# Optimization experiments

Measured on AMD Instinct MI355X. Metric: run time of the kernel, lower is better.

## Reference

```python
import jax, jax.numpy as jnp
import numpy as np

N_NODES = 100000
N_EDGES = 1600000
IN_C, HID_C, OUT_C = 256, 128, 64


def sage_conv(x, src, dst, Wl, Wr, b, n_nodes):
    """PyG SAGEConv: lin_l(mean of neighbor messages) + lin_r(x) + b."""
    msgs = x[src]  # [E, C] gather
    agg = jax.ops.segment_sum(msgs, dst, num_segments=n_nodes)  # [N, C] scatter-add
    deg = jax.ops.segment_sum(jnp.ones((src.shape[0],), x.dtype), dst, num_segments=n_nodes)
    agg = agg / jnp.maximum(deg, 1.0)[:, None]  # mean aggregation, safe for isolated nodes
    return agg @ Wl + x @ Wr + b


def setup_inputs() -> dict:
    key = jax.random.key(0)
    ks = jax.random.split(key, 12)

    def glorot(k, shape):
        fan_in, fan_out = shape
        lim = float(np.sqrt(6.0 / (fan_in + fan_out)))
        return jax.random.uniform(k, shape, jnp.float32, -lim, lim)

    x = jax.random.normal(ks[0], (N_NODES, IN_C), jnp.float32)
    edge_index = jax.random.randint(ks[1], (2, N_EDGES), 0, N_NODES, jnp.int32)
    return {
        "x": x,
        "edge_index": edge_index,
        "Wl0": glorot(ks[2], (IN_C, HID_C)),
        "Wr0": glorot(ks[3], (IN_C, HID_C)),
        "b0": jnp.zeros((HID_C,), jnp.float32),
        "Wl1": glorot(ks[4], (HID_C, HID_C)),
        "Wr1": glorot(ks[5], (HID_C, HID_C)),
        "b1": jnp.zeros((HID_C,), jnp.float32),
        "Wl2": glorot(ks[6], (HID_C, OUT_C)),
        "Wr2": glorot(ks[7], (HID_C, OUT_C)),
        "b2": jnp.zeros((OUT_C,), jnp.float32),
    }


def reference(x, edge_index, Wl0, Wr0, b0, Wl1, Wr1, b1, Wl2, Wr2, b2):
    src, dst = edge_index[0], edge_index[1]
    n = x.shape[0]
    h = x
    out = None
    # convs[:-1]: conv -> relu -> dropout (eval mode: dropout = identity)
    for Wl, Wr, b in ((Wl0, Wr0, b0), (Wl1, Wr1, b1)):
        out = sage_conv(h, src, dst, Wl, Wr, b, n)
        h = jax.nn.relu(out)
    g = h
    x_final = sage_conv(g, src, dst, Wl2, Wr2, b2, n)
    return (x_final, out, g)
```

## Files before the change

kernel.cpp:

```cpp
#include <hip/hip_runtime.h>
#include <stdint.h>

typedef __attribute__((ext_vector_type(4))) float f32x4;
typedef _Float16 half8 __attribute__((ext_vector_type(8)));
typedef _Float16 half4 __attribute__((ext_vector_type(4)));


#define BIN_CHUNK 8192
#define MAXB 512

__global__ __launch_bounds__(256) void k_bhist(const int* __restrict__ dst,
                                               int* __restrict__ bcnt, int E) {
    __shared__ int lh[MAXB];
    for (int i = threadIdx.x; i < MAXB; i += 256) lh[i] = 0;
    __syncthreads();
    const int base = blockIdx.x * BIN_CHUNK;
#pragma unroll 4
    for (int i = 0; i < BIN_CHUNK / 256; i++) {
        int e = base + i * 256 + threadIdx.x;
        if (e < E) atomicAdd(&lh[dst[e] >> 8], 1);
    }
    __syncthreads();
    for (int i = threadIdx.x; i < MAXB; i += 256)
        if (lh[i]) atomicAdd(&bcnt[i], lh[i]);
}

__global__ __launch_bounds__(512) void k_pscan(const int* __restrict__ in,
                                               int* __restrict__ out0,
                                               int* __restrict__ out1,
                                               int* __restrict__ tot, int n) {
    __shared__ int sh[512];
    const int t = threadIdx.x;
    int v[4];
    int s = 0;
#pragma unroll
    for (int i = 0; i < 4; i++) {
        int idx = t * 4 + i;
        v[i] = (idx < n) ? in[idx] : 0;
        s += v[i];
    }
    sh[t] = s;
    __syncthreads();
    for (int off = 1; off < 512; off <<= 1) {
        int add = (t >= off) ? sh[t - off] : 0;
        __syncthreads();
        sh[t] += add;
        __syncthreads();
    }
    int excl = sh[t] - s;
#pragma unroll
    for (int i = 0; i < 4; i++) {
        int idx = t * 4 + i;
        if (idx < n) {
            out0[idx] = excl;
            if (out1) out1[idx] = excl;
        }
        excl += v[i];
    }
    if (t == 511 && tot) *tot = sh[511];
}

__global__ __launch_bounds__(256) void k_bin(const int* __restrict__ src,
                                             const int* __restrict__ dst,
                                             int* __restrict__ gcur,
                                             unsigned* __restrict__ ebuf, int E) {
    __shared__ int lh[MAXB];
    __shared__ int lcur[MAXB];
    for (int i = threadIdx.x; i < MAXB; i += 256) lh[i] = 0;
    __syncthreads();
    const int base = blockIdx.x * BIN_CHUNK;
#pragma unroll 4
    for (int i = 0; i < BIN_CHUNK / 256; i++) {
        int e = base + i * 256 + threadIdx.x;
        if (e < E) atomicAdd(&lh[dst[e] >> 8], 1);
    }
    __syncthreads();
    for (int i = threadIdx.x; i < MAXB; i += 256)
        lcur[i] = lh[i] ? atomicAdd(&gcur[i], lh[i]) : 0;
    __syncthreads();
#pragma unroll 4
    for (int i = 0; i < BIN_CHUNK / 256; i++) {
        int e = base + i * 256 + threadIdx.x;
        if (e < E) {
            int d = dst[e];
            int pos = atomicAdd(&lcur[d >> 8], 1);
            ebuf[pos] = (unsigned)src[e] | ((unsigned)(d & 255) << 24);
        }
    }
}

__global__ __launch_bounds__(256) void k_csr(const unsigned* __restrict__ ebuf,
                                             const int* __restrict__ bbase,
                                             int* __restrict__ rowptr,
                                             int* __restrict__ ssrc, int N) {
    __shared__ int cnt[256];
    __shared__ int sh[256];
    __shared__ int lc[256];
    const int t = threadIdx.x;
    const int b = blockIdx.x;
    cnt[t] = 0;
    __syncthreads();
    const int lo = bbase[b], hi = bbase[b + 1];
    for (int e = lo + t; e < hi; e += 256)
        atomicAdd(&cnt[ebuf[e] >> 24], 1);
    __syncthreads();
    const int myc = cnt[t];
    sh[t] = myc;
    __syncthreads();
    for (int off = 1; off < 256; off <<= 1) {
        int add = (t >= off) ? sh[t - off] : 0;
        __syncthreads();
        sh[t] += add;
        __syncthreads();
    }
    const int base = lo + (sh[t] - myc);
    const int n = (b << 8) + t;
    if (n <= N) rowptr[n] = base;
    lc[t] = base;
    __syncthreads();
    for (int e = lo + t; e < hi; e += 256) {
        unsigned v = ebuf[e];
        int pos = atomicAdd(&lc[v >> 24], 1);
        ssrc[pos] = (int)(v & 0xFFFFFFu);
    }
}


template <int K, int NCOLT>
__device__ inline void wprep_one(const float* __restrict__ Wl, const float* __restrict__ Wr,
                                 _Float16* __restrict__ Wt, int i) {
    constexpr int NCOL = NCOLT / 2;
    int n = i / K, k = i - n * K;
    float v = (n < NCOL) ? Wl[(size_t)k * NCOL + n] : Wr[(size_t)k * NCOL + (n - NCOL)];
    Wt[(size_t)(k >> 5) * (NCOLT * 32) + n * 32 + (k & 31)] = (_Float16)v;
}

__global__ __launch_bounds__(256) void k_wprepAll(
    const float* __restrict__ Wl0, const float* __restrict__ Wr0,
    const float* __restrict__ Wl1, const float* __restrict__ Wr1,
    const float* __restrict__ Wl2, const float* __restrict__ Wr2,
    _Float16* __restrict__ Wt0, _Float16* __restrict__ Wt1, _Float16* __restrict__ Wt2) {
    int i = blockIdx.x * 256 + threadIdx.x;
    if (i < 65536) wprep_one<256, 256>(Wl0, Wr0, Wt0, i);
    else if (i < 98304) wprep_one<128, 256>(Wl1, Wr1, Wt1, i - 65536);
    else if (i < 114688) wprep_one<128, 128>(Wl2, Wr2, Wt2, i - 98304);
}


template <int K, int NCOLT, bool AF32>
__global__ __launch_bounds__(256) void k_gemmM(const void* __restrict__ Av,
                                               const _Float16* __restrict__ Wt,
                                               const float* __restrict__ bias,
                                               _Float16* __restrict__ Cl,
                                               _Float16* __restrict__ Cr, int M) {
    constexpr int NCOL = NCOLT / 2;
    constexpr int WC = NCOLT / 4;
    constexpr int NT = WC / 16;
    constexpr int AS = K + 8;
    constexpr int CS = NCOLT + 8;
    constexpr int MAXS = (K > NCOLT ? K : NCOLT) + 8;
    __shared__ _Float16 sh[64 * MAXS];

    const int tid = threadIdx.x;
    const int lane = tid & 63;
    const int wave = tid >> 6;
    const int quad = lane >> 4;
    const int l16 = lane & 15;
    const int m0 = blockIdx.x * 64;
    const int colbase = wave * WC;

    if (AF32) {
        const float* A = (const float*)Av;
#pragma unroll
        for (int i = 0; i < K / 16; i++) {
            int off = i * 1024 + tid * 4;
            int row = off / K, col = off % K;
            f32x4 u = {0.f, 0.f, 0.f, 0.f};
            if (m0 + row < M) u = *(const f32x4*)(A + (size_t)(m0 + row) * K + col);
            half4 h = {(_Float16)u[0], (_Float16)u[1], (_Float16)u[2], (_Float16)u[3]};
            *(half4*)(sh + row * AS + col) = h;
        }
    } else {
        const _Float16* A = (const _Float16*)Av;
#pragma unroll
        for (int i = 0; i < K / 32; i++) {
            int off = i * 2048 + tid * 8;
            int row = off / K, col = off % K;
            half8 u = {0, 0, 0, 0, 0, 0, 0, 0};
            if (m0 + row < M) u = *(const half8*)(A + (size_t)(m0 + row) * K + col);
            *(half8*)(sh + row * AS + col) = u;
        }
    }
    __syncthreads();

    f32x4 acc[4][NT];
#pragma unroll
    for (int rg = 0; rg < 4; rg++)
#pragma unroll
        for (int t = 0; t < NT; t++) acc[rg][t] = (f32x4){0.f, 0.f, 0.f, 0.f};

#pragma unroll
    for (int k0 = 0; k0 < K; k0 += 32) {
        half8 a[4];
#pragma unroll
        for (int rg = 0; rg < 4; rg++)
            a[rg] = *(const half8*)(sh + (rg * 16 + l16) * AS + k0 + quad * 8);
        half8 b[NT];
        const _Float16* Wk = Wt + (size_t)(k0 >> 5) * (NCOLT * 32);
#pragma unroll
        for (int t = 0; t < NT; t++)
            b[t] = *(const half8*)(Wk + (colbase + t * 16 + l16) * 32 + quad * 8);
#pragma unroll
        for (int rg = 0; rg < 4; rg++)
#pragma unroll
            for (int t = 0; t < NT; t++)
                acc[rg][t] = __builtin_amdgcn_mfma_f32_16x16x32_f16(b[t], a[rg], acc[rg][t], 0, 0, 0);
    }

    __syncthreads();

#pragma unroll
    for (int t = 0; t < NT; t++) {
        int c0 = colbase + t * 16 + quad * 4;
        f32x4 bv = {0.f, 0.f, 0.f, 0.f};
        if (c0 >= NCOL) bv = *(const f32x4*)(bias + (c0 - NCOL));
#pragma unroll
        for (int rg = 0; rg < 4; rg++) {
            half4 h = {(_Float16)(acc[rg][t][0] + bv[0]), (_Float16)(acc[rg][t][1] + bv[1]),
                       (_Float16)(acc[rg][t][2] + bv[2]), (_Float16)(acc[rg][t][3] + bv[3])};
            *(half4*)(sh + (rg * 16 + l16) * CS + c0) = h;
        }
    }
    __syncthreads();

#pragma unroll
    for (int i = 0; i < (64 * NCOL) / 2048; i++) {
        int off = i * 2048 + tid * 8;
        int row = off / NCOL, col = off % NCOL;
        if (m0 + row < M) {
            *(half8*)(Cl + (size_t)(m0 + row) * NCOL + col) = *(const half8*)(sh + row * CS + col);
            *(half8*)(Cr + (size_t)(m0 + row) * NCOL + col) = *(const half8*)(sh + row * CS + NCOL + col);
        }
    }
}


template <int COUT, int MODE>
__global__ __launch_bounds__(256) void k_agg(const half8* __restrict__ xl,
                                             const half8* __restrict__ xr,
                                             const int* __restrict__ rowptr,
                                             const int* __restrict__ ssrc,
                                             float* __restrict__ outF1,
                                             float* __restrict__ outF2,
                                             _Float16* __restrict__ outH, int N) {
    constexpr int LPN = COUT / 16;
    constexpr int NPB = 256 / LPN;
    constexpr int C8 = COUT / 8;
    const int tid = threadIdx.x;
    const int c = tid % LPN;
    const int n = blockIdx.x * NPB + tid / LPN;
    if (n >= N) return;

    const int rp0 = rowptr[n];
    const int rp1 = rowptr[n + 1];
    float acc[16];
#pragma unroll
    for (int i = 0; i < 16; i++) acc[i] = 0.f;

    const size_t cb = (size_t)c * 2;
    int e = rp0;
    for (; e + 7 < rp1; e += 8) {
        int s[8];
#pragma unroll
        for (int u = 0; u < 8; u++) s[u] = ssrc[e + u];
        half8 va[8], vb[8];
#pragma unroll
        for (int u = 0; u < 8; u++) {
            const half8* p = xl + (size_t)s[u] * C8 + cb;
            va[u] = p[0];
            vb[u] = p[1];
        }
#pragma unroll
        for (int u = 0; u < 8; u++)
#pragma unroll
            for (int i = 0; i < 8; i++) {
                acc[i] += (float)va[u][i];
                acc[8 + i] += (float)vb[u][i];
            }
    }
    for (; e + 3 < rp1; e += 4) {
        int s0 = ssrc[e], s1 = ssrc[e + 1], s2 = ssrc[e + 2], s3 = ssrc[e + 3];
        half8 v0a = xl[(size_t)s0 * C8 + cb], v0b = xl[(size_t)s0 * C8 + cb + 1];
        half8 v1a = xl[(size_t)s1 * C8 + cb], v1b = xl[(size_t)s1 * C8 + cb + 1];
        half8 v2a = xl[(size_t)s2 * C8 + cb], v2b = xl[(size_t)s2 * C8 + cb + 1];
        half8 v3a = xl[(size_t)s3 * C8 + cb], v3b = xl[(size_t)s3 * C8 + cb + 1];
#pragma unroll
        for (int i = 0; i < 8; i++) {
            acc[i] += (float)v0a[i] + (float)v1a[i] + (float)v2a[i] + (float)v3a[i];
            acc[8 + i] += (float)v0b[i] + (float)v1b[i] + (float)v2b[i] + (float)v3b[i];
        }
    }
    for (; e < rp1; e++) {
        int s = ssrc[e];
        half8 va = xl[(size_t)s * C8 + cb], vb = xl[(size_t)s * C8 + cb + 1];
#pragma unroll
        for (int i = 0; i < 8; i++) {
            acc[i] += (float)va[i];
            acc[8 + i] += (float)vb[i];
        }
    }

    const int deg = rp1 - rp0;
    const float scale = 1.0f / (float)(deg > 1 ? deg : 1);
    half8 x0 = xr[(size_t)n * C8 + cb];
    half8 x1 = xr[(size_t)n * C8 + cb + 1];
    float res[16];
#pragma unroll
    for (int i = 0; i < 8; i++) {
        res[i] = acc[i] * scale + (float)x0[i];
        res[8 + i] = acc[8 + i] * scale + (float)x1[i];
    }

    const size_t ob = (size_t)n * COUT + (size_t)c * 16;
    if (MODE == 0) {
        half8 h0v, h1v;
#pragma unroll
        for (int i = 0; i < 8; i++) {
            h0v[i] = (_Float16)(res[i] > 0.f ? res[i] : 0.f);
            h1v[i] = (_Float16)(res[8 + i] > 0.f ? res[8 + i] : 0.f);
        }
        *(half8*)(outH + ob) = h0v;
        *(half8*)(outH + ob + 8) = h1v;
    } else if (MODE == 1) {
#pragma unroll
        for (int q = 0; q < 4; q++) {
            f32x4 v = {res[q * 4], res[q * 4 + 1], res[q * 4 + 2], res[q * 4 + 3]};
            *(f32x4*)(outF1 + ob + q * 4) = v;
            f32x4 z = {v[0] > 0.f ? v[0] : 0.f, v[1] > 0.f ? v[1] : 0.f,
                       v[2] > 0.f ? v[2] : 0.f, v[3] > 0.f ? v[3] : 0.f};
            *(f32x4*)(outF2 + ob + q * 4) = z;
        }
        half8 h0v, h1v;
#pragma unroll
        for (int i = 0; i < 8; i++) {
            h0v[i] = (_Float16)(res[i] > 0.f ? res[i] : 0.f);
            h1v[i] = (_Float16)(res[8 + i] > 0.f ? res[8 + i] : 0.f);
        }
        *(half8*)(outH + ob) = h0v;
        *(half8*)(outH + ob + 8) = h1v;
    } else {
#pragma unroll
        for (int q = 0; q < 4; q++) {
            f32x4 v = {res[q * 4], res[q * 4 + 1], res[q * 4 + 2], res[q * 4 + 3]};
            *(f32x4*)(outF1 + ob + q * 4) = v;
        }
    }
}


extern "C" void kernel_launch(void* const* d_in, const int* in_sizes, int n_in,
                              void* d_out, int out_size, void* d_ws, size_t ws_size,
                              hipStream_t stream) {
    const float* x   = (const float*)d_in[0];
    const int*   ei  = (const int*)d_in[1];
    const float* Wl0 = (const float*)d_in[2];
    const float* Wr0 = (const float*)d_in[3];
    const float* b0  = (const float*)d_in[4];
    const float* Wl1 = (const float*)d_in[5];
    const float* Wr1 = (const float*)d_in[6];
    const float* b1  = (const float*)d_in[7];
    const float* Wl2 = (const float*)d_in[8];
    const float* Wr2 = (const float*)d_in[9];
    const float* b2  = (const float*)d_in[10];

    const int N = in_sizes[0] / 256;
    const int E = in_sizes[1] / 2;
    const int* src = ei;
    const int* dst = ei + E;

    char* p = (char*)d_ws;
    auto alloc = [&](size_t bytes) -> void* {
        void* r = (void*)p;
        p += (bytes + 255) & ~(size_t)255;
        return r;
    };
    int*      rowptr   = (int*)alloc((size_t)(N + 1) * 4);
    int*      bcnt     = (int*)alloc(MAXB * 4);
    int*      bbase    = (int*)alloc((MAXB + 1) * 4);
    int*      gcur     = (int*)alloc(MAXB * 4);
    int*      ssrc     = (int*)alloc((size_t)E * 4);
    _Float16* xl       = (_Float16*)alloc((size_t)N * 128 * 2);
    _Float16* xr       = (_Float16*)alloc((size_t)N * 128 * 2);
    _Float16* h0       = (_Float16*)alloc((size_t)N * 128 * 2);
    _Float16* gb       = (_Float16*)alloc((size_t)N * 128 * 2);
    _Float16* Wt0      = (_Float16*)alloc((size_t)256 * 256 * 2);
    _Float16* Wt1      = (_Float16*)alloc((size_t)256 * 128 * 2);
    _Float16* Wt2      = (_Float16*)alloc((size_t)128 * 128 * 2);

    unsigned* ebuf = (unsigned*)gb;

    float* out = (float*)d_out;
    float* x_final = out;
    float* out1    = out + (size_t)N * 64;
    float* g       = out + (size_t)N * 192;

    const int nb = (N + 255) >> 8;
    const int nbk = (E + BIN_CHUNK - 1) / BIN_CHUNK;

    hipMemsetAsync(bcnt, 0, MAXB * 4, stream);
    k_bhist<<<nbk, 256, 0, stream>>>(dst, bcnt, E);
    k_pscan<<<1, 512, 0, stream>>>(bcnt, bbase, gcur, bbase + nb, nb);
    k_bin<<<nbk, 256, 0, stream>>>(src, dst, gcur, ebuf, E);
    k_csr<<<nb, 256, 0, stream>>>(ebuf, bbase, rowptr, ssrc, N);

    k_wprepAll<<<448, 256, 0, stream>>>(Wl0, Wr0, Wl1, Wr1, Wl2, Wr2, Wt0, Wt1, Wt2);

    const int gGrid = (N + 63) / 64;

    k_gemmM<256, 256, true><<<gGrid, 256, 0, stream>>>(x, Wt0, b0, xl, xr, N);
    k_agg<128, 0><<<(N + 31) / 32, 256, 0, stream>>>((const half8*)xl, (const half8*)xr,
                                                     rowptr, ssrc, nullptr, nullptr, h0, N);

    k_gemmM<128, 256, false><<<gGrid, 256, 0, stream>>>(h0, Wt1, b1, xl, xr, N);
    k_agg<128, 1><<<(N + 31) / 32, 256, 0, stream>>>((const half8*)xl, (const half8*)xr,
                                                     rowptr, ssrc, out1, g, gb, N);

    k_gemmM<128, 128, false><<<gGrid, 256, 0, stream>>>(gb, Wt2, b2, xl, xr, N);
    k_agg<64, 2><<<(N + 63) / 64, 256, 0, stream>>>((const half8*)xl, (const half8*)xr,
                                                    rowptr, ssrc, x_final, nullptr, nullptr, N);
}
```

Before: 536.5 us.

## Merge weight prep into histogram and first GEMM into binning kernel

Weight transposition and fp16 conversion now run as extra blocks of the histogram kernel, and the first-layer GEMM runs as extra blocks of the edge binning kernel. Independent work therefore shares one launch and can overlap, and two launches are removed. The 8-way unrolled gather loop in the aggregation kernel is also dropped in favour of the 4-way loop. The binning blocks now reserve the GEMM's larger shared-memory footprint, which may reduce their occupancy.

```diff
diff --git a/kernel.cpp b/kernel.cpp
--- a/kernel.cpp
+++ b/kernel.cpp
@@ -9,20 +9,41 @@
 #define BIN_CHUNK 8192
 #define MAXB 512
 
-__global__ __launch_bounds__(256) void k_bhist(const int* __restrict__ dst,
-                                               int* __restrict__ bcnt, int E) {
-    __shared__ int lh[MAXB];
-    for (int i = threadIdx.x; i < MAXB; i += 256) lh[i] = 0;
-    __syncthreads();
-    const int base = blockIdx.x * BIN_CHUNK;
+
+template <int K, int NCOLT>
+__device__ inline void wprep_one(const float* __restrict__ Wl, const float* __restrict__ Wr,
+                                 _Float16* __restrict__ Wt, int i) {
+    constexpr int NCOL = NCOLT / 2;
+    int n = i / K, k = i - n * K;
+    float v = (n < NCOL) ? Wl[(size_t)k * NCOL + n] : Wr[(size_t)k * NCOL + (n - NCOL)];
+    Wt[(size_t)(k >> 5) * (NCOLT * 32) + n * 32 + (k & 31)] = (_Float16)v;
+}
+
+__global__ __launch_bounds__(256) void k_bhistW(
+    const int* __restrict__ dst, int* __restrict__ bcnt, int E, int nbk,
+    const float* __restrict__ Wl0, const float* __restrict__ Wr0,
+    const float* __restrict__ Wl1, const float* __restrict__ Wr1,
+    const float* __restrict__ Wl2, const float* __restrict__ Wr2,
+    _Float16* __restrict__ Wt0, _Float16* __restrict__ Wt1, _Float16* __restrict__ Wt2) {
+    if ((int)blockIdx.x < nbk) {
+        __shared__ int lh[MAXB];
+        for (int i = threadIdx.x; i < MAXB; i += 256) lh[i] = 0;
+        __syncthreads();
+        const int base = blockIdx.x * BIN_CHUNK;
 #pragma unroll 4
-    for (int i = 0; i < BIN_CHUNK / 256; i++) {
-        int e = base + i * 256 + threadIdx.x;
-        if (e < E) atomicAdd(&lh[dst[e] >> 8], 1);
-    }
-    __syncthreads();
-    for (int i = threadIdx.x; i < MAXB; i += 256)
-        if (lh[i]) atomicAdd(&bcnt[i], lh[i]);
+        for (int i = 0; i < BIN_CHUNK / 256; i++) {
+            int e = base + i * 256 + threadIdx.x;
+            if (e < E) atomicAdd(&lh[dst[e] >> 8], 1);
+        }
+        __syncthreads();
+        for (int i = threadIdx.x; i < MAXB; i += 256)
+            if (lh[i]) atomicAdd(&bcnt[i], lh[i]);
+    } else {
+        int i = (blockIdx.x - nbk) * 256 + threadIdx.x;
+        if (i < 65536) wprep_one<256, 256>(Wl0, Wr0, Wt0, i);
+        else if (i < 98304) wprep_one<128, 256>(Wl1, Wr1, Wt1, i - 65536);
+        else if (i < 114688) wprep_one<128, 128>(Wl2, Wr2, Wt2, i - 98304);
+    }
 }
 
 __global__ __launch_bounds__(512) void k_pscan(const int* __restrict__ in,
@@ -60,15 +81,15 @@
     if (t == 511 && tot) *tot = sh[511];
 }
 
-__global__ __launch_bounds__(256) void k_bin(const int* __restrict__ src,
-                                             const int* __restrict__ dst,
-                                             int* __restrict__ gcur,
-                                             unsigned* __restrict__ ebuf, int E) {
-    __shared__ int lh[MAXB];
-    __shared__ int lcur[MAXB];
+
+__device__ inline void bin_body(const int* __restrict__ src, const int* __restrict__ dst,
+                                int* __restrict__ gcur, unsigned* __restrict__ ebuf,
+                                int E, int bid, int* __restrict__ smem) {
+    int* lh = smem;
+    int* lcur = smem + MAXB;
     for (int i = threadIdx.x; i < MAXB; i += 256) lh[i] = 0;
     __syncthreads();
-    const int base = blockIdx.x * BIN_CHUNK;
+    const int base = bid * BIN_CHUNK;
 #pragma unroll 4
     for (int i = 0; i < BIN_CHUNK / 256; i++) {
         int e = base + i * 256 + threadIdx.x;
@@ -86,6 +107,129 @@
             int pos = atomicAdd(&lcur[d >> 8], 1);
             ebuf[pos] = (unsigned)src[e] | ((unsigned)(d & 255) << 24);
         }
+    }
+}
+
+
+template <int K, int NCOLT, bool AF32>
+__device__ inline void gemm_body(const void* __restrict__ Av,
+                                 const _Float16* __restrict__ Wt,
+                                 const float* __restrict__ bias,
+                                 _Float16* __restrict__ Cl,
+                                 _Float16* __restrict__ Cr, int M, int bid,
+                                 _Float16* __restrict__ sh) {
+    constexpr int NCOL = NCOLT / 2;
+    constexpr int WC = NCOLT / 4;
+    constexpr int NT = WC / 16;
+    constexpr int AS = K + 8;
+    constexpr int CS = NCOLT + 8;
+
+    const int tid = threadIdx.x;
+    const int lane = tid & 63;
+    const int wave = tid >> 6;
+    const int quad = lane >> 4;
+    const int l16 = lane & 15;
+    const int m0 = bid * 64;
+    const int colbase = wave * WC;
+
+    if (AF32) {
+        const float* A = (const float*)Av;
+#pragma unroll
+        for (int i = 0; i < K / 16; i++) {
+            int off = i * 1024 + tid * 4;
+            int row = off / K, col = off % K;
+            f32x4 u = {0.f, 0.f, 0.f, 0.f};
+            if (m0 + row < M) u = *(const f32x4*)(A + (size_t)(m0 + row) * K + col);
+            half4 h = {(_Float16)u[0], (_Float16)u[1], (_Float16)u[2], (_Float16)u[3]};
+            *(half4*)(sh + row * AS + col) = h;
+        }
+    } else {
+        const _Float16* A = (const _Float16*)Av;
+#pragma unroll
+        for (int i = 0; i < K / 32; i++) {
+            int off = i * 2048 + tid * 8;
+            int row = off / K, col = off % K;
+            half8 u = {0, 0, 0, 0, 0, 0, 0, 0};
+            if (m0 + row < M) u = *(const half8*)(A + (size_t)(m0 + row) * K + col);
+            *(half8*)(sh + row * AS + col) = u;
+        }
+    }
+    __syncthreads();
+
+    f32x4 acc[4][NT];
+#pragma unroll
+    for (int rg = 0; rg < 4; rg++)
+#pragma unroll
+        for (int t = 0; t < NT; t++) acc[rg][t] = (f32x4){0.f, 0.f, 0.f, 0.f};
+
+#pragma unroll
+    for (int k0 = 0; k0 < K; k0 += 32) {
+        half8 a[4];
+#pragma unroll
+        for (int rg = 0; rg < 4; rg++)
+            a[rg] = *(const half8*)(sh + (rg * 16 + l16) * AS + k0 + quad * 8);
+        half8 b[NT];
+        const _Float16* Wk = Wt + (size_t)(k0 >> 5) * (NCOLT * 32);
+#pragma unroll
+        for (int t = 0; t < NT; t++)
+            b[t] = *(const half8*)(Wk + (colbase + t * 16 + l16) * 32 + quad * 8);
+#pragma unroll
+        for (int rg = 0; rg < 4; rg++)
+#pragma unroll
+            for (int t = 0; t < NT; t++)
+                acc[rg][t] = __builtin_amdgcn_mfma_f32_16x16x32_f16(b[t], a[rg], acc[rg][t], 0, 0, 0);
+    }
+
+    __syncthreads();
+
+#pragma unroll
+    for (int t = 0; t < NT; t++) {
+        int c0 = colbase + t * 16 + quad * 4;
+        f32x4 bv = {0.f, 0.f, 0.f, 0.f};
+        if (c0 >= NCOL) bv = *(const f32x4*)(bias + (c0 - NCOL));
+#pragma unroll
+        for (int rg = 0; rg < 4; rg++) {
+            half4 h = {(_Float16)(acc[rg][t][0] + bv[0]), (_Float16)(acc[rg][t][1] + bv[1]),
+                       (_Float16)(acc[rg][t][2] + bv[2]), (_Float16)(acc[rg][t][3] + bv[3])};
+            *(half4*)(sh + (rg * 16 + l16) * CS + c0) = h;
+        }
+    }
+    __syncthreads();
+
+#pragma unroll
+    for (int i = 0; i < (64 * NCOL) / 2048; i++) {
+        int off = i * 2048 + tid * 8;
+        int row = off / NCOL, col = off % NCOL;
+        if (m0 + row < M) {
+            *(half8*)(Cl + (size_t)(m0 + row) * NCOL + col) = *(const half8*)(sh + row * CS + col);
+            *(half8*)(Cr + (size_t)(m0 + row) * NCOL + col) = *(const half8*)(sh + row * CS + NCOL + col);
+        }
+    }
+}
+
+template <int K, int NCOLT, bool AF32>
+__global__ __launch_bounds__(256) void k_gemmM(const void* __restrict__ Av,
+                                               const _Float16* __restrict__ Wt,
+                                               const float* __restrict__ bias,
+                                               _Float16* __restrict__ Cl,
+                                               _Float16* __restrict__ Cr, int M) {
+    constexpr int MAXS = (K > NCOLT ? K : NCOLT) + 8;
+    __shared__ _Float16 sh[64 * MAXS];
+    gemm_body<K, NCOLT, AF32>(Av, Wt, bias, Cl, Cr, M, blockIdx.x, sh);
+}
+
+__global__ __launch_bounds__(256) void k_binGemm0(
+    const int* __restrict__ src, const int* __restrict__ dst,
+    int* __restrict__ gcur, unsigned* __restrict__ ebuf, int E, int nbk,
+    const float* __restrict__ x, const _Float16* __restrict__ Wt0,
+    const float* __restrict__ b0, _Float16* __restrict__ xl,
+    _Float16* __restrict__ xr, int M) {
+    __shared__ __align__(16) char smem[64 * 264 * 2];
+    if ((int)blockIdx.x < nbk) {
+        bin_body(src, dst, gcur, ebuf, E, blockIdx.x, (int*)smem);
+    } else {
+        gemm_body<256, 256, true>(x, Wt0, b0, xl, xr, M, blockIdx.x - nbk,
+                                  (_Float16*)smem);
     }
 }
 
@@ -122,125 +266,6 @@
         unsigned v = ebuf[e];
         int pos = atomicAdd(&lc[v >> 24], 1);
         ssrc[pos] = (int)(v & 0xFFFFFFu);
-    }
-}
-
-
-template <int K, int NCOLT>
-__device__ inline void wprep_one(const float* __restrict__ Wl, const float* __restrict__ Wr,
-                                 _Float16* __restrict__ Wt, int i) {
-    constexpr int NCOL = NCOLT / 2;
-    int n = i / K, k = i - n * K;
-    float v = (n < NCOL) ? Wl[(size_t)k * NCOL + n] : Wr[(size_t)k * NCOL + (n - NCOL)];
-    Wt[(size_t)(k >> 5) * (NCOLT * 32) + n * 32 + (k & 31)] = (_Float16)v;
-}
-
-__global__ __launch_bounds__(256) void k_wprepAll(
-    const float* __restrict__ Wl0, const float* __restrict__ Wr0,
-    const float* __restrict__ Wl1, const float* __restrict__ Wr1,
-    const float* __restrict__ Wl2, const float* __restrict__ Wr2,
-    _Float16* __restrict__ Wt0, _Float16* __restrict__ Wt1, _Float16* __restrict__ Wt2) {
-    int i = blockIdx.x * 256 + threadIdx.x;
-    if (i < 65536) wprep_one<256, 256>(Wl0, Wr0, Wt0, i);
-    else if (i < 98304) wprep_one<128, 256>(Wl1, Wr1, Wt1, i - 65536);
-    else if (i < 114688) wprep_one<128, 128>(Wl2, Wr2, Wt2, i - 98304);
-}
-
-
-template <int K, int NCOLT, bool AF32>
-__global__ __launch_bounds__(256) void k_gemmM(const void* __restrict__ Av,
-                                               const _Float16* __restrict__ Wt,
-                                               const float* __restrict__ bias,
-                                               _Float16* __restrict__ Cl,
-                                               _Float16* __restrict__ Cr, int M) {
-    constexpr int NCOL = NCOLT / 2;
-    constexpr int WC = NCOLT / 4;
-    constexpr int NT = WC / 16;
-    constexpr int AS = K + 8;
-    constexpr int CS = NCOLT + 8;
-    constexpr int MAXS = (K > NCOLT ? K : NCOLT) + 8;
-    __shared__ _Float16 sh[64 * MAXS];
-
-    const int tid = threadIdx.x;
-    const int lane = tid & 63;
-    const int wave = tid >> 6;
-    const int quad = lane >> 4;
-    const int l16 = lane & 15;
-    const int m0 = blockIdx.x * 64;
-    const int colbase = wave * WC;
-
-    if (AF32) {
-        const float* A = (const float*)Av;
-#pragma unroll
-        for (int i = 0; i < K / 16; i++) {
-            int off = i * 1024 + tid * 4;
-            int row = off / K, col = off % K;
-            f32x4 u = {0.f, 0.f, 0.f, 0.f};
-            if (m0 + row < M) u = *(const f32x4*)(A + (size_t)(m0 + row) * K + col);
-            half4 h = {(_Float16)u[0], (_Float16)u[1], (_Float16)u[2], (_Float16)u[3]};
-            *(half4*)(sh + row * AS + col) = h;
-        }
-    } else {
-        const _Float16* A = (const _Float16*)Av;
-#pragma unroll
-        for (int i = 0; i < K / 32; i++) {
-            int off = i * 2048 + tid * 8;
-            int row = off / K, col = off % K;
-            half8 u = {0, 0, 0, 0, 0, 0, 0, 0};
-            if (m0 + row < M) u = *(const half8*)(A + (size_t)(m0 + row) * K + col);
-            *(half8*)(sh + row * AS + col) = u;
-        }
-    }
-    __syncthreads();
-
-    f32x4 acc[4][NT];
-#pragma unroll
-    for (int rg = 0; rg < 4; rg++)
-#pragma unroll
-        for (int t = 0; t < NT; t++) acc[rg][t] = (f32x4){0.f, 0.f, 0.f, 0.f};
-
-#pragma unroll
-    for (int k0 = 0; k0 < K; k0 += 32) {
-        half8 a[4];
-#pragma unroll
-        for (int rg = 0; rg < 4; rg++)
-            a[rg] = *(const half8*)(sh + (rg * 16 + l16) * AS + k0 + quad * 8);
-        half8 b[NT];
-        const _Float16* Wk = Wt + (size_t)(k0 >> 5) * (NCOLT * 32);
-#pragma unroll
-        for (int t = 0; t < NT; t++)
-            b[t] = *(const half8*)(Wk + (colbase + t * 16 + l16) * 32 + quad * 8);
-#pragma unroll
-        for (int rg = 0; rg < 4; rg++)
-#pragma unroll
-            for (int t = 0; t < NT; t++)
-                acc[rg][t] = __builtin_amdgcn_mfma_f32_16x16x32_f16(b[t], a[rg], acc[rg][t], 0, 0, 0);
-    }
-
-    __syncthreads();
-
-#pragma unroll
-    for (int t = 0; t < NT; t++) {
-        int c0 = colbase + t * 16 + quad * 4;
-        f32x4 bv = {0.f, 0.f, 0.f, 0.f};
-        if (c0 >= NCOL) bv = *(const f32x4*)(bias + (c0 - NCOL));
-#pragma unroll
-        for (int rg = 0; rg < 4; rg++) {
-            half4 h = {(_Float16)(acc[rg][t][0] + bv[0]), (_Float16)(acc[rg][t][1] + bv[1]),
-                       (_Float16)(acc[rg][t][2] + bv[2]), (_Float16)(acc[rg][t][3] + bv[3])};
-            *(half4*)(sh + (rg * 16 + l16) * CS + c0) = h;
-        }
-    }
-    __syncthreads();
-
-#pragma unroll
-    for (int i = 0; i < (64 * NCOL) / 2048; i++) {
-        int off = i * 2048 + tid * 8;
-        int row = off / NCOL, col = off % NCOL;
-        if (m0 + row < M) {
-            *(half8*)(Cl + (size_t)(m0 + row) * NCOL + col) = *(const half8*)(sh + row * CS + col);
-            *(half8*)(Cr + (size_t)(m0 + row) * NCOL + col) = *(const half8*)(sh + row * CS + NCOL + col);
-        }
     }
 }
 
@@ -269,25 +294,6 @@
 
     const size_t cb = (size_t)c * 2;
     int e = rp0;
-    for (; e + 7 < rp1; e += 8) {
-        int s[8];
-#pragma unroll
-        for (int u = 0; u < 8; u++) s[u] = ssrc[e + u];
-        half8 va[8], vb[8];
-#pragma unroll
-        for (int u = 0; u < 8; u++) {
-            const half8* p = xl + (size_t)s[u] * C8 + cb;
-            va[u] = p[0];
-            vb[u] = p[1];
-        }
-#pragma unroll
-        for (int u = 0; u < 8; u++)
-#pragma unroll
-            for (int i = 0; i < 8; i++) {
-                acc[i] += (float)va[u][i];
-                acc[8 + i] += (float)vb[u][i];
-            }
-    }
     for (; e + 3 < rp1; e += 4) {
         int s0 = ssrc[e], s1 = ssrc[e + 1], s2 = ssrc[e + 2], s3 = ssrc[e + 3];
         half8 v0a = xl[(size_t)s0 * C8 + cb], v0b = xl[(size_t)s0 * C8 + cb + 1];
@@ -406,18 +412,17 @@
 
     const int nb = (N + 255) >> 8;
     const int nbk = (E + BIN_CHUNK - 1) / BIN_CHUNK;
+    const int gGrid = (N + 63) / 64;
 
     hipMemsetAsync(bcnt, 0, MAXB * 4, stream);
-    k_bhist<<<nbk, 256, 0, stream>>>(dst, bcnt, E);
+    k_bhistW<<<nbk + 448, 256, 0, stream>>>(dst, bcnt, E, nbk,
+                                            Wl0, Wr0, Wl1, Wr1, Wl2, Wr2,
+                                            Wt0, Wt1, Wt2);
     k_pscan<<<1, 512, 0, stream>>>(bcnt, bbase, gcur, bbase + nb, nb);
-    k_bin<<<nbk, 256, 0, stream>>>(src, dst, gcur, ebuf, E);
+    k_binGemm0<<<nbk + gGrid, 256, 0, stream>>>(src, dst, gcur, ebuf, E, nbk,
+                                                x, Wt0, b0, xl, xr, N);
     k_csr<<<nb, 256, 0, stream>>>(ebuf, bbase, rowptr, ssrc, N);
 
-    k_wprepAll<<<448, 256, 0, stream>>>(Wl0, Wr0, Wl1, Wr1, Wl2, Wr2, Wt0, Wt1, Wt2);
-
-    const int gGrid = (N + 63) / 64;
-
-    k_gemmM<256, 256, true><<<gGrid, 256, 0, stream>>>(x, Wt0, b0, xl, xr, N);
     k_agg<128, 0><<<(N + 31) / 32, 256, 0, stream>>>((const half8*)xl, (const half8*)xr,
                                                      rowptr, ssrc, nullptr, nullptr, h0, N);
 
```

Result: faster. 513.6 us (-4.3%).
